# Kernel optimization log

Measured on AMD Instinct MI355X. Metric: run time of the kernel, lower is better.

Reference implementation:

```python
import jax, jax.numpy as jnp
import numpy as np

HIDDEN = 2048
HEADS = 16
HEAD_DIM = HIDDEN // HEADS          # 128
KV_RANK = HIDDEN // 8               # 256 (kv_compression_ratio = 8)
ATTN_DIM = HEADS * HEAD_DIM         # 2048
EPS = 1e-6


def setup_inputs() -> dict:
    key = jax.random.key(0)
    ks = jax.random.split(key, 6)
    B, L = 2, 2048
    x = jax.random.normal(ks[0], (B, L, HIDDEN), dtype=jnp.float32)
    # weights stored [in, out] (torch Linear applies x @ W.T; same math)
    s = lambda fan_in: 1.0 / np.sqrt(fan_in)
    Wq = jax.random.normal(ks[1], (HIDDEN, ATTN_DIM), dtype=jnp.float32) * s(HIDDEN)
    Wkv_down = jax.random.normal(ks[2], (HIDDEN, KV_RANK), dtype=jnp.float32) * s(HIDDEN)
    kv_norm_w = jnp.ones((KV_RANK,), dtype=jnp.float32)
    Wkv_up = jax.random.normal(ks[3], (KV_RANK, 2 * ATTN_DIM), dtype=jnp.float32) * s(KV_RANK)
    Wo = jax.random.normal(ks[4], (ATTN_DIM, HIDDEN), dtype=jnp.float32) * s(ATTN_DIM)
    return {"x": x, "Wq": Wq, "Wkv_down": Wkv_down, "kv_norm_w": kv_norm_w,
            "Wkv_up": Wkv_up, "Wo": Wo}


def rms_norm(x, w):
    ms = jnp.mean(x * x, axis=-1, keepdims=True)
    return w * (x * jax.lax.rsqrt(ms + EPS))


def reference(x, Wq, Wkv_down, kv_norm_w, Wkv_up, Wo):
    B, L, D = x.shape
    q = (x @ Wq).reshape(B, L, HEADS, HEAD_DIM)
    latent = rms_norm(x @ Wkv_down, kv_norm_w)            # [B, L, KV_RANK]
    kv = latent @ Wkv_up                                   # [B, L, 2*ATTN_DIM]
    k, v = jnp.split(kv, 2, axis=-1)
    k = k.reshape(B, L, HEADS, HEAD_DIM)
    v = v.reshape(B, L, HEADS, HEAD_DIM)
    scores = jnp.einsum('bxhd,byhd->bhxy', q, k) / np.sqrt(HEAD_DIM)
    causal = jnp.tril(jnp.ones((L, L), dtype=bool))
    scores = jnp.where(causal, scores, -jnp.inf)
    attn = jax.nn.softmax(scores, axis=-1)
    out = jnp.einsum('bhxy,byhd->bxhd', attn, v).reshape(B, L, ATTN_DIM)
    return out @ Wo
```

## Files before the change

### kernel.cpp

```cpp
#include <hip/hip_runtime.h>
#include <cstdint>
#include <cstddef>

typedef unsigned short u16;
typedef __bf16 bf16x8 __attribute__((ext_vector_type(8)));
typedef __bf16 bf16x2 __attribute__((ext_vector_type(2)));
typedef float f32x4 __attribute__((ext_vector_type(4)));
typedef uint32_t u32x4 __attribute__((ext_vector_type(4)));

__device__ inline u16 f2bf(float f) {
  uint32_t u = __builtin_bit_cast(uint32_t, f);
  u += 0x7fffu + ((u >> 16) & 1u);
  return (u16)(u >> 16);
}

#if defined(__has_builtin)
#if __has_builtin(__builtin_amdgcn_cvt_pk_bf16_f32)
#define HAVE_PK_BF16 1
#endif
#if __has_builtin(__builtin_amdgcn_exp2f)
#define EXP2(x) __builtin_amdgcn_exp2f(x)
#endif
#endif
#ifndef EXP2
#define EXP2(x) exp2f(x)
#endif

__device__ inline uint32_t pk2bf(float a, float b) {
#ifdef HAVE_PK_BF16
  bf16x2 v = __builtin_amdgcn_cvt_pk_bf16_f32(a, b);
  return __builtin_bit_cast(uint32_t, v);
#else
  return (uint32_t)f2bf(a) | ((uint32_t)f2bf(b) << 16);
#endif
}

__device__ inline f32x4 mfma16(bf16x8 a, bf16x8 b, f32x4 c) {
  return __builtin_amdgcn_mfma_f32_16x16x32_bf16(a, b, c, 0, 0, 0);
}

__device__ inline void gl_lds16(const u16* g, u16* l) {
  __builtin_amdgcn_global_load_lds(
      (const __attribute__((address_space(1))) uint32_t*)g,
      (__attribute__((address_space(3))) uint32_t*)l, 16, 0, 0);
}

__device__ void tcvt_dev(const float* __restrict__ in, u16* __restrict__ out,
                         int R, int C, int bx, int by, float (*t)[33], int tid) {
  int cb = bx * 32, rb = by * 32;
  int x = tid & 31, y = tid >> 5;
#pragma unroll
  for (int k = 0; k < 4; ++k)
    t[y + k * 8][x] = in[(size_t)(rb + y + k * 8) * C + cb + x];
  __syncthreads();
#pragma unroll
  for (int k = 0; k < 4; ++k)
    out[(size_t)(cb + y + k * 8) * R + rb + x] = f2bf(t[x][y + k * 8]);
}

__global__ __launch_bounds__(256) void k_prep(
    const float* __restrict__ x, const float* __restrict__ Wq,
    const float* __restrict__ Wkvd, const float* __restrict__ Wkvu,
    const float* __restrict__ Wo, u16* __restrict__ xbf,
    u16* __restrict__ WqkdT, u16* __restrict__ WkvuT, u16* __restrict__ WoT) {
  __shared__ float t[32][33];
  int bid = blockIdx.x, tid = threadIdx.x;
  if (bid < 8192) {
    int i = bid * 256 + tid;
    const float4 v = ((const float4*)x)[i];
    ushort4 o;
    o.x = f2bf(v.x); o.y = f2bf(v.y); o.z = f2bf(v.z); o.w = f2bf(v.w);
    ((ushort4*)xbf)[i] = o;
  } else if (bid < 12288) {
    int q = bid - 8192;
    tcvt_dev(Wq, WqkdT, 2048, 2048, q & 63, q >> 6, t, tid);
  } else if (bid < 12800) {
    int q = bid - 12288;
    tcvt_dev(Wkvd, WqkdT + 2048 * 2048, 2048, 256, q & 7, q >> 3, t, tid);
  } else if (bid < 13824) {
    int q = bid - 12800;
    tcvt_dev(Wkvu, WkvuT, 256, 4096, q & 127, q >> 7, t, tid);
  } else {
    int q = bid - 13824;
    tcvt_dev(Wo, WoT, 2048, 2048, q & 63, q >> 6, t, tid);
  }
}

__global__ __launch_bounds__(256) void k_rmsn(const u16* __restrict__ qc,
                                              const float* __restrict__ w,
                                              u16* __restrict__ out) {
  int row = blockIdx.x * 4 + (threadIdx.x >> 6);
  int lane = threadIdx.x & 63;
  const ushort4 u = *(const ushort4*)(qc + (size_t)row * 2304 + 2048 + lane * 4);
  float4 v;
  v.x = __builtin_bit_cast(float, (uint32_t)u.x << 16);
  v.y = __builtin_bit_cast(float, (uint32_t)u.y << 16);
  v.z = __builtin_bit_cast(float, (uint32_t)u.z << 16);
  v.w = __builtin_bit_cast(float, (uint32_t)u.w << 16);
  float ss = v.x * v.x + v.y * v.y + v.z * v.z + v.w * v.w;
#pragma unroll
  for (int off = 1; off < 64; off <<= 1) ss += __shfl_xor(ss, off);
  float r = rsqrtf(ss * (1.f / 256.f) + 1e-6f);
  const float4 wv = ((const float4*)w)[lane];
  ushort4 o;
  o.x = f2bf(v.x * r * wv.x);
  o.y = f2bf(v.y * r * wv.y);
  o.z = f2bf(v.z * r * wv.z);
  o.w = f2bf(v.w * r * wv.w);
  *(ushort4*)(out + (size_t)row * 256 + lane * 4) = o;
}

template <int BK, int MODE>
__global__ __launch_bounds__(256) void k_gemm(const u16* __restrict__ A,
                                              const u16* __restrict__ BT,
                                              void* __restrict__ C,
                                              u16* __restrict__ C2, int K,
                                              int ldc, float scale) {
  __shared__ __align__(16) u16 As[128 * BK];
  __shared__ __align__(16) u16 Bs[128 * BK];
  const int tid = threadIdx.x, wave = tid >> 6, lane = tid & 63;
  const int lanem = lane & 15, quad = lane >> 4;
  const int m0 = blockIdx.x * 128, n0 = blockIdx.y * 128;
  const int wr = wave >> 1, wc = wave & 1;
  f32x4 acc[4][4] = {};
  for (int k0 = 0; k0 < K; k0 += BK) {
    __syncthreads();
    if constexpr (BK == 32) {
      const int srow = lane >> 2, scol = (lane & 3) * 8;
#pragma unroll
      for (int c = 0; c < 2; ++c) {
        int p = wave * 2 + c;
        gl_lds16(A + (size_t)(m0 + p * 16 + srow) * K + k0 + scol, &As[p * 512]);
        gl_lds16(BT + (size_t)(n0 + p * 16 + srow) * K + k0 + scol, &Bs[p * 512]);
      }
    } else {
      const int srow = lane >> 3;
      const int scol = ((lane & 7) ^ srow) * 8;
#pragma unroll
      for (int c = 0; c < 4; ++c) {
        int p = wave * 4 + c;
        gl_lds16(A + (size_t)(m0 + p * 8 + srow) * K + k0 + scol, &As[p * 512]);
        gl_lds16(BT + (size_t)(n0 + p * 8 + srow) * K + k0 + scol, &Bs[p * 512]);
      }
    }
    __syncthreads();
#pragma unroll
    for (int kk = 0; kk < BK / 32; ++kk) {
      bf16x8 af[4], bff[4];
      if constexpr (BK == 32) {
#pragma unroll
        for (int i = 0; i < 4; ++i)
          af[i] = *(const bf16x8*)&As[(wr * 64 + i * 16 + lanem) * 32 + quad * 8];
#pragma unroll
        for (int j = 0; j < 4; ++j)
          bff[j] = *(const bf16x8*)&Bs[(wc * 64 + j * 16 + lanem) * 32 + quad * 8];
      } else {
        const int kp = ((kk * 4 + quad) ^ (lanem & 7)) << 3;
#pragma unroll
        for (int i = 0; i < 4; ++i)
          af[i] = *(const bf16x8*)&As[(wr * 64 + i * 16 + lanem) * 64 + kp];
#pragma unroll
        for (int j = 0; j < 4; ++j)
          bff[j] = *(const bf16x8*)&Bs[(wc * 64 + j * 16 + lanem) * 64 + kp];
      }
#pragma unroll
      for (int i = 0; i < 4; ++i)
#pragma unroll
        for (int j = 0; j < 4; ++j)
          acc[i][j] = mfma16(af[i], bff[j], acc[i][j]);
    }
  }
#pragma unroll
  for (int i = 0; i < 4; ++i)
#pragma unroll
    for (int j = 0; j < 4; ++j) {
      const int row0 = m0 + wr * 64 + i * 16 + quad * 4;
      const int col = n0 + wc * 64 + j * 16 + lanem;
      if constexpr (MODE == 2) {
        if (col >= 2048) {
          int cc = col - 2048, hh = cc >> 7, dd = cc & 127;
          int bb = row0 >> 11, ll = row0 & 2047;
          ushort4 pk;
          pk.x = f2bf(acc[i][j][0]);
          pk.y = f2bf(acc[i][j][1]);
          pk.z = f2bf(acc[i][j][2]);
          pk.w = f2bf(acc[i][j][3]);
          *(ushort4*)&C2[((size_t)(bb * 16 + hh) * 128 + dd) * 2048 + ll] = pk;
          continue;
        }
      }
#pragma unroll
      for (int r = 0; r < 4; ++r) {
        float v = acc[i][j][r] * scale;
        if constexpr (MODE == 0)
          ((float*)C)[(size_t)(row0 + r) * ldc + col] = v;
        else if constexpr (MODE == 1)
          ((u16*)C)[(size_t)(row0 + r) * ldc + col] = f2bf(v);
        else
          ((u16*)C)[(size_t)(row0 + r) * 2048 + col] = f2bf(v);
      }
    }
}

__global__ __launch_bounds__(256) void k_attn(const u16* __restrict__ qg,
                                              const u16* __restrict__ kg,
                                              const u16* __restrict__ vtg,
                                              u16* __restrict__ ao) {
  __shared__ __align__(16) u16 Ks[2][64 * 128];
  __shared__ __align__(16) u16 VTs[2][144 * 64];
  const int bid = blockIdx.x;
  const int p = bid >> 5, u = bid & 31;
  const int qt = (bid < 256) ? (15 - p) : (p - 8);
  const int bh = (u & 7) * 4 + (u >> 3);
  const int b = bh >> 4, h = bh & 15;
  const int tid = threadIdx.x, w = tid >> 6, lane = tid & 63;
  const int lanem = lane & 15, quad = lane >> 4;
  const int qb = qt * 128, nt = 2 * qt + 2;

  const int kr = lane >> 4, kc = lane & 15;
  const u16* kbp[4];
#pragma unroll
  for (int j = 0; j < 4; ++j) {
    int key = ((w >> 1) << 5) + (j << 3) + ((w & 1) << 2) + kr;
    kbp[j] = kg + (size_t)(b * 2048 + key) * 2048 + h * 128 +
             ((kc ^ (j * 4 + kr)) << 3);
  }
  const int vr = lane >> 3, vc = lane & 7;
  const u16* vbp[4];
#pragma unroll
  for (int j = 0; j < 4; ++j) {
    int row = w * 32 + j * 8 + vr;
    vbp[j] = vtg + (size_t)(bh * 128 + row) * 2048 + ((vc ^ vr) << 3);
  }

  bf16x8 qf[2][4];
#pragma unroll
  for (int g = 0; g < 2; ++g) {
    const u16* qp = qg +
                    (size_t)(b * 2048 + qb + w * 32 + g * 16 + lanem) * 2304 +
                    h * 128 + quad * 8;
#pragma unroll
    for (int c = 0; c < 4; ++c) qf[g][c] = *(const bf16x8*)(qp + c * 32);
  }
  f32x4 o[2][9] = {};

  int kpc[4], vposc[2];
#pragma unroll
  for (int c = 0; c < 4; ++c) kpc[c] = ((c * 4 + quad) ^ lanem) << 3;
#pragma unroll
  for (int kk = 0; kk < 2; ++kk)
    vposc[kk] = ((kk * 4 + quad) ^ (lanem & 7)) << 3;

#pragma unroll
  for (int j = 0; j < 4; ++j) gl_lds16(kbp[j], &Ks[0][(w * 16 + j * 4) * 128]);
#pragma unroll
  for (int j = 0; j < 4; ++j) gl_lds16(vbp[j], &VTs[0][(w * 32 + j * 8) * 64]);
#pragma unroll
  for (int j = 0; j < 4; ++j) { kbp[j] += 64 * 2048; vbp[j] += 64; }
  {
    const ushort4 ones4{0x3f80u, 0x3f80u, 0x3f80u, 0x3f80u};
    for (int i = tid; i < 512; i += 256) {
      int bufi = i >> 8, off = (i & 255) * 4;
      *(ushort4*)&VTs[bufi][128 * 64 + off] = ones4;
    }
  }

  for (int t = 0; t < nt; ++t) {
    __syncthreads();
    if (t + 1 < nt) {
      int nb = (t + 1) & 1;
#pragma unroll
      for (int j = 0; j < 4; ++j)
        gl_lds16(kbp[j], &Ks[nb][(w * 16 + j * 4) * 128]);
#pragma unroll
      for (int j = 0; j < 4; ++j)
        gl_lds16(vbp[j], &VTs[nb][(w * 32 + j * 8) * 64]);
#pragma unroll
      for (int j = 0; j < 4; ++j) { kbp[j] += 64 * 2048; vbp[j] += 64; }
    }
    const int buf = t & 1;
    const u16* ksb = &Ks[buf][lanem * 128];
    const u16* vsb = &VTs[buf][lanem * 64];
    f32x4 s[2][4] = {};
#pragma unroll
    for (int c = 0; c < 4; ++c) {
      const u16* ka = ksb + kpc[c];
#pragma unroll
      for (int ss = 0; ss < 4; ++ss) {
        bf16x8 kf = *(const bf16x8*)(ka + ss * 2048);
        s[0][ss] = mfma16(kf, qf[0][c], s[0][ss]);
        s[1][ss] = mfma16(kf, qf[1][c], s[1][ss]);
      }
    }
    if (t >= nt - 2) {
      const int krel = t * 64 - qb;
#pragma unroll
      for (int g = 0; g < 2; ++g) {
        const int qrow = w * 32 + g * 16 + lanem;
#pragma unroll
        for (int ss = 0; ss < 4; ++ss) {
          const int kb0 = krel + ((ss & 2) << 4) + ((ss & 1) << 2) + (quad << 3);
#pragma unroll
          for (int r = 0; r < 4; ++r)
            if (kb0 + r > qrow) s[g][ss][r] = -1e30f;
        }
      }
    }
    bf16x8 pf[2][2];
#pragma unroll
    for (int g = 0; g < 2; ++g)
#pragma unroll
      for (int f = 0; f < 2; ++f) {
        u32x4 pw;
        pw.x = pk2bf(EXP2(s[g][2 * f][0]), EXP2(s[g][2 * f][1]));
        pw.y = pk2bf(EXP2(s[g][2 * f][2]), EXP2(s[g][2 * f][3]));
        pw.z = pk2bf(EXP2(s[g][2 * f + 1][0]), EXP2(s[g][2 * f + 1][1]));
        pw.w = pk2bf(EXP2(s[g][2 * f + 1][2]), EXP2(s[g][2 * f + 1][3]));
        pf[g][f] = __builtin_bit_cast(bf16x8, pw);
      }
#pragma unroll
    for (int dc = 0; dc < 9; ++dc) {
      const u16* va = vsb + dc * 1024;
      bf16x8 vf0 = *(const bf16x8*)(va + vposc[0]);
      bf16x8 vf1 = *(const bf16x8*)(va + vposc[1]);
      o[0][dc] = mfma16(pf[0][0], vf0, o[0][dc]);
      o[0][dc] = mfma16(pf[0][1], vf1, o[0][dc]);
      o[1][dc] = mfma16(pf[1][0], vf0, o[1][dc]);
      o[1][dc] = mfma16(pf[1][1], vf1, o[1][dc]);
    }
  }
#pragma unroll
  for (int g = 0; g < 2; ++g)
#pragma unroll
    for (int r = 0; r < 4; ++r) {
      const float inv = 1.f / o[g][8][r];
      u16* op = ao +
                (size_t)(b * 2048 + qb + w * 32 + g * 16 + quad * 4 + r) * 2048 +
                h * 128;
#pragma unroll
      for (int dc = 0; dc < 8; ++dc)
        op[dc * 16 + lanem] = f2bf(o[g][dc][r] * inv);
    }
}

extern "C" void kernel_launch(void* const* d_in, const int* in_sizes, int n_in,
                              void* d_out, int out_size, void* d_ws, size_t ws_size,
                              hipStream_t stream) {
  const float* x    = (const float*)d_in[0];
  const float* Wq   = (const float*)d_in[1];
  const float* Wkvd = (const float*)d_in[2];
  const float* wn   = (const float*)d_in[3];
  const float* Wkvu = (const float*)d_in[4];
  const float* Wo   = (const float*)d_in[5];
  float* out = (float*)d_out;

  char* w0 = (char*)d_ws;
  u16* xbf   = (u16*)(w0);
  u16* qc    = (u16*)(w0 + 16777216);
  u16* WqkdT = (u16*)(w0 + 35651584);
  u16* WoT   = (u16*)(w0 + 45088768);
  u16* WkvuT = (u16*)(w0 + 53477376);
  u16* kbf   = (u16*)(w0 + 55574528);
  u16* vtbf  = (u16*)(w0 + 72351744);
  u16* latbf = WqkdT;
  u16* aobf  = xbf;

  const float sc2 = 0.08838834764831845f * 1.4426950408889634f;

  k_prep<<<17920, 256, 0, stream>>>(x, Wq, Wkvd, Wkvu, Wo, xbf, WqkdT, WkvuT, WoT);
  k_gemm<32, 1><<<dim3(32, 18), 256, 0, stream>>>(xbf, WqkdT, qc, nullptr, 2048,
                                                  2304, sc2);
  k_rmsn<<<1024, 256, 0, stream>>>(qc, wn, latbf);
  k_gemm<64, 2><<<dim3(32, 32), 256, 0, stream>>>(latbf, WkvuT, kbf, vtbf, 256,
                                                  0, 1.0f);
  k_attn<<<512, 256, 0, stream>>>(qc, kbf, vtbf, aobf);
  k_gemm<32, 0><<<dim3(32, 16), 256, 0, stream>>>(aobf, WoT, out, nullptr, 2048,
                                                  2048, 1.0f);
}
```

Before: 314.3 us.

## Split long causal attention query tiles across two key ranges with reduction kernel

The attention kernel now splits each of the 8 longest query tiles (qt 8..15) into two blocks that cover separate halves of the key range. Each half writes unnormalized fp32 partial outputs and row sums to a workspace, and a new reduction kernel adds them and normalizes into the bf16 attention output. This is meant to balance the load across CUs, since the longest causal tiles set the critical path of the 512-block grid. In exchange it adds a second launch and an fp32 partial write and read. The split path is used only if the workspace is large enough.

After: 326.5 us. 3.9% more time.

```diff
diff --git a/kernel.cpp b/kernel.cpp
--- a/kernel.cpp
+++ b/kernel.cpp
@@ -202,16 +202,43 @@
     }
 }
 
+template <bool SPLIT>
 __global__ __launch_bounds__(256) void k_attn(const u16* __restrict__ qg,
                                               const u16* __restrict__ kg,
                                               const u16* __restrict__ vtg,
-                                              u16* __restrict__ ao) {
+                                              u16* __restrict__ ao,
+                                              float* __restrict__ OP,
+                                              float* __restrict__ LP) {
   __shared__ __align__(16) u16 Ks[2][64 * 128];
   __shared__ __align__(16) u16 VTs[2][144 * 64];
   const int bid = blockIdx.x;
-  const int p = bid >> 5, u = bid & 31;
-  const int qt = (bid < 256) ? (15 - p) : (p - 8);
-  const int bh = (u & 7) * 4 + (u >> 3);
+  int qt, bh, ts, te, ck = 0;
+  bool part = false;
+  if constexpr (SPLIT) {
+    if (bid < 512) {
+      qt = 15 - (bid >> 6);
+      const int rem = bid & 63;
+      ck = rem & 1;
+      const int uu = rem >> 1;
+      bh = (uu & 7) * 4 + (uu >> 3);
+      ts = ck ? (qt + 1) : 0;
+      te = ck ? (2 * qt + 2) : (qt + 1);
+      part = true;
+    } else {
+      const int idx = bid - 512;
+      qt = 7 - (idx >> 5);
+      const int u = idx & 31;
+      bh = (u & 7) * 4 + (u >> 3);
+      ts = 0;
+      te = 2 * qt + 2;
+    }
+  } else {
+    const int p = bid >> 5, u = bid & 31;
+    qt = (bid < 256) ? (15 - p) : (p - 8);
+    bh = (u & 7) * 4 + (u >> 3);
+    ts = 0;
+    te = 2 * qt + 2;
+  }
   const int b = bh >> 4, h = bh & 15;
   const int tid = threadIdx.x, w = tid >> 6, lane = tid & 63;
   const int lanem = lane & 15, quad = lane >> 4;
@@ -223,14 +250,15 @@
   for (int j = 0; j < 4; ++j) {
     int key = ((w >> 1) << 5) + (j << 3) + ((w & 1) << 2) + kr;
     kbp[j] = kg + (size_t)(b * 2048 + key) * 2048 + h * 128 +
-             ((kc ^ (j * 4 + kr)) << 3);
+             ((kc ^ (j * 4 + kr)) << 3) + (size_t)ts * 64 * 2048;
   }
   const int vr = lane >> 3, vc = lane & 7;
   const u16* vbp[4];
 #pragma unroll
   for (int j = 0; j < 4; ++j) {
     int row = w * 32 + j * 8 + vr;
-    vbp[j] = vtg + (size_t)(bh * 128 + row) * 2048 + ((vc ^ vr) << 3);
+    vbp[j] = vtg + (size_t)(bh * 128 + row) * 2048 + ((vc ^ vr) << 3) +
+             (size_t)ts * 64;
   }
 
   bf16x8 qf[2][4];
@@ -265,10 +293,10 @@
     }
   }
 
-  for (int t = 0; t < nt; ++t) {
+  for (int t = ts; t < te; ++t) {
     __syncthreads();
-    if (t + 1 < nt) {
-      int nb = (t + 1) & 1;
+    if (t + 1 < te) {
+      int nb = (t + 1 - ts) & 1;
 #pragma unroll
       for (int j = 0; j < 4; ++j)
         gl_lds16(kbp[j], &Ks[nb][(w * 16 + j * 4) * 128]);
@@ -278,7 +306,7 @@
 #pragma unroll
       for (int j = 0; j < 4; ++j) { kbp[j] += 64 * 2048; vbp[j] += 64; }
     }
-    const int buf = t & 1;
+    const int buf = (t - ts) & 1;
     const u16* ksb = &Ks[buf][lanem * 128];
     const u16* vsb = &VTs[buf][lanem * 64];
     f32x4 s[2][4] = {};
@@ -329,18 +357,63 @@
       o[1][dc] = mfma16(pf[1][1], vf1, o[1][dc]);
     }
   }
-#pragma unroll
-  for (int g = 0; g < 2; ++g)
-#pragma unroll
-    for (int r = 0; r < 4; ++r) {
-      const float inv = 1.f / o[g][8][r];
-      u16* op = ao +
-                (size_t)(b * 2048 + qb + w * 32 + g * 16 + quad * 4 + r) * 2048 +
-                h * 128;
-#pragma unroll
-      for (int dc = 0; dc < 8; ++dc)
-        op[dc * 16 + lanem] = f2bf(o[g][dc][r] * inv);
-    }
+  if (SPLIT && part) {
+    const int slot = ((qt - 8) * 32 + bh) * 2 + ck;
+    float* op = OP + (size_t)slot * 16384;
+#pragma unroll
+    for (int g = 0; g < 2; ++g)
+#pragma unroll
+      for (int r = 0; r < 4; ++r) {
+        const int row = w * 32 + g * 16 + quad * 4 + r;
+#pragma unroll
+        for (int dc = 0; dc < 8; ++dc)
+          op[row * 128 + dc * 16 + lanem] = o[g][dc][r];
+        if (lanem == 0) LP[slot * 128 + row] = o[g][8][r];
+      }
+  } else {
+#pragma unroll
+    for (int g = 0; g < 2; ++g)
+#pragma unroll
+      for (int r = 0; r < 4; ++r) {
+        const float inv = 1.f / o[g][8][r];
+        u16* op = ao +
+                  (size_t)(b * 2048 + qb + w * 32 + g * 16 + quad * 4 + r) * 2048 +
+                  h * 128;
+#pragma unroll
+        for (int dc = 0; dc < 8; ++dc)
+          op[dc * 16 + lanem] = f2bf(o[g][dc][r] * inv);
+      }
+  }
+}
+
+__global__ __launch_bounds__(256) void k_ared(const float* __restrict__ OP,
+                                              const float* __restrict__ LP,
+                                              u16* __restrict__ ao) {
+  __shared__ float linv[128];
+  const int sp = blockIdx.x;
+  const int qt = 8 + (sp >> 5), bh = sp & 31;
+  const int b = bh >> 4, h = bh & 15;
+  const int tid = threadIdx.x;
+  if (tid < 128)
+    linv[tid] = 1.f / (LP[sp * 256 + tid] + LP[sp * 256 + 128 + tid]);
+  __syncthreads();
+  const float4* pa = (const float4*)(OP + (size_t)sp * 32768);
+  const float4* pb = pa + 4096;
+  u16* abase = ao + (size_t)(b * 2048 + qt * 128) * 2048 + h * 128;
+#pragma unroll
+  for (int k = 0; k < 16; ++k) {
+    const int fi = k * 256 + tid;
+    const int row = fi >> 5, dd = (fi & 31) * 4;
+    const float4 va = pa[fi];
+    const float4 vb = pb[fi];
+    const float inv = linv[row];
+    ushort4 o4;
+    o4.x = f2bf((va.x + vb.x) * inv);
+    o4.y = f2bf((va.y + vb.y) * inv);
+    o4.z = f2bf((va.z + vb.z) * inv);
+    o4.w = f2bf((va.w + vb.w) * inv);
+    *(ushort4*)(abase + (size_t)row * 2048 + dd) = o4;
+  }
 }
 
 extern "C" void kernel_launch(void* const* d_in, const int* in_sizes, int n_in,
@@ -365,6 +438,13 @@
   u16* latbf = WqkdT;
   u16* aobf  = xbf;
 
+  const size_t PBOFF = 89128960;
+  const size_t OPSZ  = 256ull * 2 * 128 * 128 * 4;
+  const size_t LPSZ  = 256ull * 2 * 128 * 4;
+  const bool do_split = ws_size >= PBOFF + OPSZ + LPSZ;
+  float* OP = (float*)(w0 + PBOFF);
+  float* LP = (float*)(w0 + PBOFF + OPSZ);
+
   const float sc2 = 0.08838834764831845f * 1.4426950408889634f;
 
   k_prep<<<17920, 256, 0, stream>>>(x, Wq, Wkvd, Wkvu, Wo, xbf, WqkdT, WkvuT, WoT);
@@ -373,7 +453,12 @@
   k_rmsn<<<1024, 256, 0, stream>>>(qc, wn, latbf);
   k_gemm<64, 2><<<dim3(32, 32), 256, 0, stream>>>(latbf, WkvuT, kbf, vtbf, 256,
                                                   0, 1.0f);
-  k_attn<<<512, 256, 0, stream>>>(qc, kbf, vtbf, aobf);
+  if (do_split) {
+    k_attn<true><<<768, 256, 0, stream>>>(qc, kbf, vtbf, aobf, OP, LP);
+    k_ared<<<256, 256, 0, stream>>>(OP, LP, aobf);
+  } else {
+    k_attn<false><<<512, 256, 0, stream>>>(qc, kbf, vtbf, aobf, nullptr, nullptr);
+  }
   k_gemm<32, 0><<<dim3(32, 16), 256, 0, stream>>>(aobf, WoT, out, nullptr, 2048,
                                                   2048, 1.0f);
 }
```

## Split causal attention along keys into two halves with a reduction kernel

Applied to the files above, without the earlier changes.

Adds a 512-thread attention kernel. Each block handles a 256-row query tile and half of the key range, and writes normalized partial outputs plus row sums to workspace. A second kernel combines the two halves weighted by their row sums. The aim is to balance the causal workload across blocks and raise occupancy, at the cost of an extra global round trip and launch. It also raises BK from 32 to 64 for the Q/latent and output GEMMs. The new path runs only when the workspace is large enough.

Result: slower. 395.2 us (+25.8%).

```diff
diff --git a/kernel.cpp b/kernel.cpp
--- a/kernel.cpp
+++ b/kernel.cpp
@@ -12,6 +12,9 @@
   uint32_t u = __builtin_bit_cast(uint32_t, f);
   u += 0x7fffu + ((u >> 16) & 1u);
   return (u16)(u >> 16);
+}
+__device__ inline float bf2f(u16 u) {
+  return __builtin_bit_cast(float, (uint32_t)u << 16);
 }
 
 #if defined(__has_builtin)
@@ -93,10 +96,7 @@
   int lane = threadIdx.x & 63;
   const ushort4 u = *(const ushort4*)(qc + (size_t)row * 2304 + 2048 + lane * 4);
   float4 v;
-  v.x = __builtin_bit_cast(float, (uint32_t)u.x << 16);
-  v.y = __builtin_bit_cast(float, (uint32_t)u.y << 16);
-  v.z = __builtin_bit_cast(float, (uint32_t)u.z << 16);
-  v.w = __builtin_bit_cast(float, (uint32_t)u.w << 16);
+  v.x = bf2f(u.x); v.y = bf2f(u.y); v.z = bf2f(u.z); v.w = bf2f(u.w);
   float ss = v.x * v.x + v.y * v.y + v.z * v.z + v.w * v.w;
 #pragma unroll
   for (int off = 1; off < 64; off <<= 1) ss += __shfl_xor(ss, off);
@@ -202,6 +202,194 @@
     }
 }
 
+__global__ __launch_bounds__(512, 4) void k_attn8(const u16* __restrict__ qg,
+                                                  const u16* __restrict__ kg,
+                                                  const u16* __restrict__ vtg,
+                                                  u16* __restrict__ OPb,
+                                                  float* __restrict__ LP) {
+  __shared__ __align__(16) u16 Ks[2][64 * 128];
+  __shared__ __align__(16) u16 VTs[2][144 * 64];
+  const int bid = blockIdx.x;
+  const int mq = (bid < 256) ? (7 - (bid >> 6)) : ((bid - 256) >> 6);
+  const int uu0 = bid & 63;
+  const int ck = uu0 & 1;
+  const int uu = uu0 >> 1;
+  const int bh = (uu & 7) * 4 + (uu >> 3);
+  const int b = bh >> 4, h = bh & 15;
+  const int ntile = 4 * mq + 4, half = 2 * mq + 2;
+  const int ts = ck ? half : 0;
+  const int te = ck ? ntile : half;
+  const int qb = mq * 256;
+
+  const int tid = threadIdx.x, w = tid >> 6, lane = tid & 63;
+  const int lanem = lane & 15, quad = lane >> 4;
+
+  const int kr = lane >> 4, kc = lane & 15;
+  const u16* kbp[2];
+  int kro[2];
+#pragma unroll
+  for (int j = 0; j < 2; ++j) {
+    const int rho = w * 8 + j * 4 + kr;
+    const int key = 32 * (rho >> 5) + 8 * ((rho >> 2) & 3) +
+                    4 * ((rho >> 4) & 1) + (rho & 3);
+    kbp[j] = kg + (size_t)(b * 2048 + key) * 2048 + h * 128 +
+             ((kc ^ (rho & 15)) << 3) + (size_t)ts * 64 * 2048;
+    kro[j] = rho * 128;
+  }
+  const int vr = lane >> 3, vc = lane & 7;
+  const u16* vbp[2];
+  int vro[2];
+#pragma unroll
+  for (int j = 0; j < 2; ++j) {
+    const int row = w * 16 + j * 8 + vr;
+    vbp[j] = vtg + (size_t)(bh * 128 + row) * 2048 + ((vc ^ vr) << 3) +
+             (size_t)ts * 64;
+    vro[j] = row * 64;
+  }
+
+  bf16x8 qf[2][4];
+#pragma unroll
+  for (int g = 0; g < 2; ++g) {
+    const u16* qp = qg +
+                    (size_t)(b * 2048 + qb + w * 32 + g * 16 + lanem) * 2304 +
+                    h * 128 + quad * 8;
+#pragma unroll
+    for (int c = 0; c < 4; ++c) qf[g][c] = *(const bf16x8*)(qp + c * 32);
+  }
+  f32x4 o[2][9] = {};
+
+  int kpc[4], vposc[2];
+#pragma unroll
+  for (int c = 0; c < 4; ++c) kpc[c] = ((c * 4 + quad) ^ lanem) << 3;
+#pragma unroll
+  for (int kk = 0; kk < 2; ++kk)
+    vposc[kk] = ((kk * 4 + quad) ^ (lanem & 7)) << 3;
+
+#pragma unroll
+  for (int j = 0; j < 2; ++j) gl_lds16(kbp[j], &Ks[0][kro[j]]);
+#pragma unroll
+  for (int j = 0; j < 2; ++j) gl_lds16(vbp[j], &VTs[0][vro[j]]);
+#pragma unroll
+  for (int j = 0; j < 2; ++j) { kbp[j] += 64 * 2048; vbp[j] += 64; }
+  {
+    const ushort4 ones4{0x3f80u, 0x3f80u, 0x3f80u, 0x3f80u};
+    const int bufi = tid >> 8, off = (tid & 255) * 4;
+    *(ushort4*)&VTs[bufi][128 * 64 + off] = ones4;
+  }
+
+  for (int t = ts; t < te; ++t) {
+    __syncthreads();
+    if (t + 1 < te) {
+      const int nb = (t + 1 - ts) & 1;
+#pragma unroll
+      for (int j = 0; j < 2; ++j) gl_lds16(kbp[j], &Ks[nb][kro[j]]);
+#pragma unroll
+      for (int j = 0; j < 2; ++j) gl_lds16(vbp[j], &VTs[nb][vro[j]]);
+#pragma unroll
+      for (int j = 0; j < 2; ++j) { kbp[j] += 64 * 2048; vbp[j] += 64; }
+    }
+    const int buf = (t - ts) & 1;
+    const u16* ksb = &Ks[buf][lanem * 128];
+    const u16* vsb = &VTs[buf][lanem * 64];
+    f32x4 s[2][4] = {};
+#pragma unroll
+    for (int c = 0; c < 4; ++c) {
+      const u16* ka = ksb + kpc[c];
+#pragma unroll
+      for (int ss = 0; ss < 4; ++ss) {
+        bf16x8 kf = *(const bf16x8*)(ka + ss * 2048);
+        s[0][ss] = mfma16(kf, qf[0][c], s[0][ss]);
+        s[1][ss] = mfma16(kf, qf[1][c], s[1][ss]);
+      }
+    }
+    if (t >= ntile - 4) {
+      const int krel = t * 64 - qb;
+#pragma unroll
+      for (int g = 0; g < 2; ++g) {
+        const int qrow = w * 32 + g * 16 + lanem;
+#pragma unroll
+        for (int ss = 0; ss < 4; ++ss) {
+          const int kb0 = krel + ((ss & 2) << 4) + ((ss & 1) << 2) + (quad << 3);
+#pragma unroll
+          for (int r = 0; r < 4; ++r)
+            if (kb0 + r > qrow) s[g][ss][r] = -1e30f;
+        }
+      }
+    }
+    bf16x8 pf[2][2];
+#pragma unroll
+    for (int g = 0; g < 2; ++g)
+#pragma unroll
+      for (int f = 0; f < 2; ++f) {
+        u32x4 pw;
+        pw.x = pk2bf(EXP2(s[g][2 * f][0]), EXP2(s[g][2 * f][1]));
+        pw.y = pk2bf(EXP2(s[g][2 * f][2]), EXP2(s[g][2 * f][3]));
+        pw.z = pk2bf(EXP2(s[g][2 * f + 1][0]), EXP2(s[g][2 * f + 1][1]));
+        pw.w = pk2bf(EXP2(s[g][2 * f + 1][2]), EXP2(s[g][2 * f + 1][3]));
+        pf[g][f] = __builtin_bit_cast(bf16x8, pw);
+      }
+#pragma unroll
+    for (int dc = 0; dc < 9; ++dc) {
+      const u16* va = vsb + dc * 1024;
+      bf16x8 vf0 = *(const bf16x8*)(va + vposc[0]);
+      bf16x8 vf1 = *(const bf16x8*)(va + vposc[1]);
+      o[0][dc] = mfma16(pf[0][0], vf0, o[0][dc]);
+      o[0][dc] = mfma16(pf[0][1], vf1, o[0][dc]);
+      o[1][dc] = mfma16(pf[1][0], vf0, o[1][dc]);
+      o[1][dc] = mfma16(pf[1][1], vf1, o[1][dc]);
+    }
+  }
+  const int slot = (mq * 32 + bh) * 2 + ck;
+  u16* opb = OPb + (size_t)slot * 32768;
+#pragma unroll
+  for (int g = 0; g < 2; ++g)
+#pragma unroll
+    for (int r = 0; r < 4; ++r) {
+      const int row = w * 32 + g * 16 + quad * 4 + r;
+      const float l = o[g][8][r];
+      const float inv = (l > 0.f) ? (1.f / l) : 0.f;
+#pragma unroll
+      for (int dc = 0; dc < 8; ++dc)
+        opb[row * 128 + dc * 16 + lanem] = f2bf(o[g][dc][r] * inv);
+      if (lanem == 0) LP[slot * 256 + row] = l;
+    }
+}
+
+__global__ __launch_bounds__(256) void k_ared2(const u16* __restrict__ OPb,
+                                               const float* __restrict__ LP,
+                                               u16* __restrict__ ao) {
+  __shared__ float2 wgt[256];
+  const int sp = blockIdx.x;
+  const int mq = sp >> 5, bh = sp & 31;
+  const int b = bh >> 4, h = bh & 15;
+  const int tid = threadIdx.x;
+  const int s0 = sp * 2, s1 = sp * 2 + 1;
+  {
+    const float l0 = LP[s0 * 256 + tid];
+    const float l1 = LP[s1 * 256 + tid];
+    const float inv = 1.f / (l0 + l1);
+    wgt[tid] = float2{l0 * inv, l1 * inv};
+  }
+  __syncthreads();
+  const ushort4* p0 = (const ushort4*)(OPb + (size_t)s0 * 32768);
+  const ushort4* p1 = (const ushort4*)(OPb + (size_t)s1 * 32768);
+  u16* abase = ao + (size_t)(b * 2048 + mq * 256) * 2048 + h * 128;
+#pragma unroll 4
+  for (int k = 0; k < 32; ++k) {
+    const int idx = k * 256 + tid;
+    const int row = idx >> 5, d4 = (idx & 31) * 4;
+    const ushort4 a4 = p0[idx];
+    const ushort4 b4 = p1[idx];
+    const float2 wv = wgt[row];
+    ushort4 o4;
+    o4.x = f2bf(bf2f(a4.x) * wv.x + bf2f(b4.x) * wv.y);
+    o4.y = f2bf(bf2f(a4.y) * wv.x + bf2f(b4.y) * wv.y);
+    o4.z = f2bf(bf2f(a4.z) * wv.x + bf2f(b4.z) * wv.y);
+    o4.w = f2bf(bf2f(a4.w) * wv.x + bf2f(b4.w) * wv.y);
+    *(ushort4*)(abase + (size_t)row * 2048 + d4) = o4;
+  }
+}
+
 __global__ __launch_bounds__(256) void k_attn(const u16* __restrict__ qg,
                                               const u16* __restrict__ kg,
                                               const u16* __restrict__ vtg,
@@ -216,7 +404,6 @@
   const int tid = threadIdx.x, w = tid >> 6, lane = tid & 63;
   const int lanem = lane & 15, quad = lane >> 4;
   const int qb = qt * 128, nt = 2 * qt + 2;
-
   const int kr = lane >> 4, kc = lane & 15;
   const u16* kbp[4];
 #pragma unroll
@@ -232,7 +419,6 @@
     int row = w * 32 + j * 8 + vr;
     vbp[j] = vtg + (size_t)(bh * 128 + row) * 2048 + ((vc ^ vr) << 3);
   }
-
   bf16x8 qf[2][4];
 #pragma unroll
   for (int g = 0; g < 2; ++g) {
@@ -243,14 +429,12 @@
     for (int c = 0; c < 4; ++c) qf[g][c] = *(const bf16x8*)(qp + c * 32);
   }
   f32x4 o[2][9] = {};
-
   int kpc[4], vposc[2];
 #pragma unroll
   for (int c = 0; c < 4; ++c) kpc[c] = ((c * 4 + quad) ^ lanem) << 3;
 #pragma unroll
   for (int kk = 0; kk < 2; ++kk)
     vposc[kk] = ((kk * 4 + quad) ^ (lanem & 7)) << 3;
-
 #pragma unroll
   for (int j = 0; j < 4; ++j) gl_lds16(kbp[j], &Ks[0][(w * 16 + j * 4) * 128]);
 #pragma unroll
@@ -264,7 +448,6 @@
       *(ushort4*)&VTs[bufi][128 * 64 + off] = ones4;
     }
   }
-
   for (int t = 0; t < nt; ++t) {
     __syncthreads();
     if (t + 1 < nt) {
@@ -365,15 +548,27 @@
   u16* latbf = WqkdT;
   u16* aobf  = xbf;
 
+  const size_t PBOFF = 89128960;
+  const size_t OPSZ  = 512ull * 256 * 128 * 2;
+  const size_t LPSZ  = 512ull * 256 * 4;
+  const bool do_split = ws_size >= PBOFF + OPSZ + LPSZ;
+  u16* OPb  = (u16*)(w0 + PBOFF);
+  float* LP = (float*)(w0 + PBOFF + OPSZ);
+
   const float sc2 = 0.08838834764831845f * 1.4426950408889634f;
 
   k_prep<<<17920, 256, 0, stream>>>(x, Wq, Wkvd, Wkvu, Wo, xbf, WqkdT, WkvuT, WoT);
-  k_gemm<32, 1><<<dim3(32, 18), 256, 0, stream>>>(xbf, WqkdT, qc, nullptr, 2048,
+  k_gemm<64, 1><<<dim3(32, 18), 256, 0, stream>>>(xbf, WqkdT, qc, nullptr, 2048,
                                                   2304, sc2);
   k_rmsn<<<1024, 256, 0, stream>>>(qc, wn, latbf);
   k_gemm<64, 2><<<dim3(32, 32), 256, 0, stream>>>(latbf, WkvuT, kbf, vtbf, 256,
                                                   0, 1.0f);
-  k_attn<<<512, 256, 0, stream>>>(qc, kbf, vtbf, aobf);
-  k_gemm<32, 0><<<dim3(32, 16), 256, 0, stream>>>(aobf, WoT, out, nullptr, 2048,
+  if (do_split) {
+    k_attn8<<<512, 512, 0, stream>>>(qc, kbf, vtbf, OPb, LP);
+    k_ared2<<<256, 256, 0, stream>>>(OPb, LP, aobf);
+  } else {
+    k_attn<<<512, 256, 0, stream>>>(qc, kbf, vtbf, aobf);
+  }
+  k_gemm<64, 0><<<dim3(32, 16), 256, 0, stream>>>(aobf, WoT, out, nullptr, 2048,
                                                   2048, 1.0f);
 }
```

## Split attention across 8 waves of 16 query rows and deepen GEMM K tiles

Applied to the files above, without the earlier changes.

The attention kernel now runs 512 threads (8 waves) per block, each wave owning 16 query rows instead of 32. Per-wave register state is halved and the K/V tile loads are spread over more threads. The aim is more waves in flight to hide LDS and exp latency, at the cost of each wave reusing every K/V fragment for fewer query rows. Separately, the Q/latent and output projection GEMMs switch from BK=32 to BK=64, cutting K-loop iterations and syncs but using more shared memory.

After: 286.0 us. 1.1x faster.

```diff
diff --git a/kernel.cpp b/kernel.cpp
--- a/kernel.cpp
+++ b/kernel.cpp
@@ -12,6 +12,9 @@
   uint32_t u = __builtin_bit_cast(uint32_t, f);
   u += 0x7fffu + ((u >> 16) & 1u);
   return (u16)(u >> 16);
+}
+__device__ inline float bf2f(u16 u) {
+  return __builtin_bit_cast(float, (uint32_t)u << 16);
 }
 
 #if defined(__has_builtin)
@@ -93,10 +96,7 @@
   int lane = threadIdx.x & 63;
   const ushort4 u = *(const ushort4*)(qc + (size_t)row * 2304 + 2048 + lane * 4);
   float4 v;
-  v.x = __builtin_bit_cast(float, (uint32_t)u.x << 16);
-  v.y = __builtin_bit_cast(float, (uint32_t)u.y << 16);
-  v.z = __builtin_bit_cast(float, (uint32_t)u.z << 16);
-  v.w = __builtin_bit_cast(float, (uint32_t)u.w << 16);
+  v.x = bf2f(u.x); v.y = bf2f(u.y); v.z = bf2f(u.z); v.w = bf2f(u.w);
   float ss = v.x * v.x + v.y * v.y + v.z * v.z + v.w * v.w;
 #pragma unroll
   for (int off = 1; off < 64; off <<= 1) ss += __shfl_xor(ss, off);
@@ -202,10 +202,10 @@
     }
 }
 
-__global__ __launch_bounds__(256) void k_attn(const u16* __restrict__ qg,
-                                              const u16* __restrict__ kg,
-                                              const u16* __restrict__ vtg,
-                                              u16* __restrict__ ao) {
+__global__ __launch_bounds__(512, 3) void k_attn16(const u16* __restrict__ qg,
+                                                   const u16* __restrict__ kg,
+                                                   const u16* __restrict__ vtg,
+                                                   u16* __restrict__ ao) {
   __shared__ __align__(16) u16 Ks[2][64 * 128];
   __shared__ __align__(16) u16 VTs[2][144 * 64];
   const int bid = blockIdx.x;
@@ -218,31 +218,31 @@
   const int qb = qt * 128, nt = 2 * qt + 2;
 
   const int kr = lane >> 4, kc = lane & 15;
-  const u16* kbp[4];
-#pragma unroll
-  for (int j = 0; j < 4; ++j) {
-    int key = ((w >> 1) << 5) + (j << 3) + ((w & 1) << 2) + kr;
+  const u16* kbp[2];
+#pragma unroll
+  for (int j = 0; j < 2; ++j) {
+    const int rho = w * 8 + j * 4 + kr;
+    const int key = 32 * (rho >> 5) + 8 * ((rho >> 2) & 3) +
+                    4 * ((rho >> 4) & 1) + (rho & 3);
     kbp[j] = kg + (size_t)(b * 2048 + key) * 2048 + h * 128 +
-             ((kc ^ (j * 4 + kr)) << 3);
+             ((kc ^ (rho & 15)) << 3);
   }
   const int vr = lane >> 3, vc = lane & 7;
-  const u16* vbp[4];
-#pragma unroll
-  for (int j = 0; j < 4; ++j) {
-    int row = w * 32 + j * 8 + vr;
+  const u16* vbp[2];
+#pragma unroll
+  for (int j = 0; j < 2; ++j) {
+    const int row = w * 16 + j * 8 + vr;
     vbp[j] = vtg + (size_t)(bh * 128 + row) * 2048 + ((vc ^ vr) << 3);
   }
 
-  bf16x8 qf[2][4];
-#pragma unroll
-  for (int g = 0; g < 2; ++g) {
-    const u16* qp = qg +
-                    (size_t)(b * 2048 + qb + w * 32 + g * 16 + lanem) * 2304 +
+  bf16x8 qf[4];
+  {
+    const u16* qp = qg + (size_t)(b * 2048 + qb + w * 16 + lanem) * 2304 +
                     h * 128 + quad * 8;
 #pragma unroll
-    for (int c = 0; c < 4; ++c) qf[g][c] = *(const bf16x8*)(qp + c * 32);
-  }
-  f32x4 o[2][9] = {};
+    for (int c = 0; c < 4; ++c) qf[c] = *(const bf16x8*)(qp + c * 32);
+  }
+  f32x4 o[9] = {};
 
   int kpc[4], vposc[2];
 #pragma unroll
@@ -252,95 +252,84 @@
     vposc[kk] = ((kk * 4 + quad) ^ (lanem & 7)) << 3;
 
 #pragma unroll
-  for (int j = 0; j < 4; ++j) gl_lds16(kbp[j], &Ks[0][(w * 16 + j * 4) * 128]);
-#pragma unroll
-  for (int j = 0; j < 4; ++j) gl_lds16(vbp[j], &VTs[0][(w * 32 + j * 8) * 64]);
-#pragma unroll
-  for (int j = 0; j < 4; ++j) { kbp[j] += 64 * 2048; vbp[j] += 64; }
+  for (int j = 0; j < 2; ++j)
+    gl_lds16(kbp[j], &Ks[0][(w * 8 + j * 4) * 128]);
+#pragma unroll
+  for (int j = 0; j < 2; ++j)
+    gl_lds16(vbp[j], &VTs[0][(w * 16 + j * 8) * 64]);
+#pragma unroll
+  for (int j = 0; j < 2; ++j) { kbp[j] += 64 * 2048; vbp[j] += 64; }
   {
     const ushort4 ones4{0x3f80u, 0x3f80u, 0x3f80u, 0x3f80u};
-    for (int i = tid; i < 512; i += 256) {
-      int bufi = i >> 8, off = (i & 255) * 4;
-      *(ushort4*)&VTs[bufi][128 * 64 + off] = ones4;
-    }
+    const int bufi = tid >> 8, off = (tid & 255) * 4;
+    *(ushort4*)&VTs[bufi][128 * 64 + off] = ones4;
   }
 
   for (int t = 0; t < nt; ++t) {
     __syncthreads();
     if (t + 1 < nt) {
-      int nb = (t + 1) & 1;
-#pragma unroll
-      for (int j = 0; j < 4; ++j)
-        gl_lds16(kbp[j], &Ks[nb][(w * 16 + j * 4) * 128]);
-#pragma unroll
-      for (int j = 0; j < 4; ++j)
-        gl_lds16(vbp[j], &VTs[nb][(w * 32 + j * 8) * 64]);
-#pragma unroll
-      for (int j = 0; j < 4; ++j) { kbp[j] += 64 * 2048; vbp[j] += 64; }
+      const int nb = (t + 1) & 1;
+#pragma unroll
+      for (int j = 0; j < 2; ++j)
+        gl_lds16(kbp[j], &Ks[nb][(w * 8 + j * 4) * 128]);
+#pragma unroll
+      for (int j = 0; j < 2; ++j)
+        gl_lds16(vbp[j], &VTs[nb][(w * 16 + j * 8) * 64]);
+#pragma unroll
+      for (int j = 0; j < 2; ++j) { kbp[j] += 64 * 2048; vbp[j] += 64; }
     }
     const int buf = t & 1;
     const u16* ksb = &Ks[buf][lanem * 128];
     const u16* vsb = &VTs[buf][lanem * 64];
-    f32x4 s[2][4] = {};
+    f32x4 s[4] = {};
 #pragma unroll
     for (int c = 0; c < 4; ++c) {
       const u16* ka = ksb + kpc[c];
 #pragma unroll
       for (int ss = 0; ss < 4; ++ss) {
         bf16x8 kf = *(const bf16x8*)(ka + ss * 2048);
-        s[0][ss] = mfma16(kf, qf[0][c], s[0][ss]);
-        s[1][ss] = mfma16(kf, qf[1][c], s[1][ss]);
+        s[ss] = mfma16(kf, qf[c], s[ss]);
       }
     }
     if (t >= nt - 2) {
       const int krel = t * 64 - qb;
-#pragma unroll
-      for (int g = 0; g < 2; ++g) {
-        const int qrow = w * 32 + g * 16 + lanem;
-#pragma unroll
-        for (int ss = 0; ss < 4; ++ss) {
-          const int kb0 = krel + ((ss & 2) << 4) + ((ss & 1) << 2) + (quad << 3);
-#pragma unroll
-          for (int r = 0; r < 4; ++r)
-            if (kb0 + r > qrow) s[g][ss][r] = -1e30f;
-        }
-      }
-    }
-    bf16x8 pf[2][2];
-#pragma unroll
-    for (int g = 0; g < 2; ++g)
-#pragma unroll
-      for (int f = 0; f < 2; ++f) {
-        u32x4 pw;
-        pw.x = pk2bf(EXP2(s[g][2 * f][0]), EXP2(s[g][2 * f][1]));
-        pw.y = pk2bf(EXP2(s[g][2 * f][2]), EXP2(s[g][2 * f][3]));
-        pw.z = pk2bf(EXP2(s[g][2 * f + 1][0]), EXP2(s[g][2 * f + 1][1]));
-        pw.w = pk2bf(EXP2(s[g][2 * f + 1][2]), EXP2(s[g][2 * f + 1][3]));
-        pf[g][f] = __builtin_bit_cast(bf16x8, pw);
-      }
+      const int qrow = w * 16 + lanem;
+#pragma unroll
+      for (int ss = 0; ss < 4; ++ss) {
+        const int kb0 = krel + ((ss & 2) << 4) + ((ss & 1) << 2) + (quad << 3);
+#pragma unroll
+        for (int r = 0; r < 4; ++r)
+          if (kb0 + r > qrow) s[ss][r] = -1e30f;
+      }
+    }
+    bf16x8 pf[2];
+#pragma unroll
+    for (int f = 0; f < 2; ++f) {
+      u32x4 pw;
+      pw.x = pk2bf(EXP2(s[2 * f][0]), EXP2(s[2 * f][1]));
+      pw.y = pk2bf(EXP2(s[2 * f][2]), EXP2(s[2 * f][3]));
+      pw.z = pk2bf(EXP2(s[2 * f + 1][0]), EXP2(s[2 * f + 1][1]));
+      pw.w = pk2bf(EXP2(s[2 * f + 1][2]), EXP2(s[2 * f + 1][3]));
+      pf[f] = __builtin_bit_cast(bf16x8, pw);
+    }
 #pragma unroll
     for (int dc = 0; dc < 9; ++dc) {
       const u16* va = vsb + dc * 1024;
       bf16x8 vf0 = *(const bf16x8*)(va + vposc[0]);
       bf16x8 vf1 = *(const bf16x8*)(va + vposc[1]);
-      o[0][dc] = mfma16(pf[0][0], vf0, o[0][dc]);
-      o[0][dc] = mfma16(pf[0][1], vf1, o[0][dc]);
-      o[1][dc] = mfma16(pf[1][0], vf0, o[1][dc]);
-      o[1][dc] = mfma16(pf[1][1], vf1, o[1][dc]);
-    }
-  }
-#pragma unroll
-  for (int g = 0; g < 2; ++g)
-#pragma unroll
-    for (int r = 0; r < 4; ++r) {
-      const float inv = 1.f / o[g][8][r];
-      u16* op = ao +
-                (size_t)(b * 2048 + qb + w * 32 + g * 16 + quad * 4 + r) * 2048 +
-                h * 128;
-#pragma unroll
-      for (int dc = 0; dc < 8; ++dc)
-        op[dc * 16 + lanem] = f2bf(o[g][dc][r] * inv);
-    }
+      o[dc] = mfma16(pf[0], vf0, o[dc]);
+      o[dc] = mfma16(pf[1], vf1, o[dc]);
+    }
+  }
+#pragma unroll
+  for (int r = 0; r < 4; ++r) {
+    const float inv = 1.f / o[8][r];
+    u16* op = ao +
+              (size_t)(b * 2048 + qb + w * 16 + quad * 4 + r) * 2048 + h * 128;
+#pragma unroll
+    for (int dc = 0; dc < 8; ++dc)
+      op[dc * 16 + lanem] = f2bf(o[dc][r] * inv);
+  }
 }
 
 extern "C" void kernel_launch(void* const* d_in, const int* in_sizes, int n_in,
@@ -368,12 +357,12 @@
   const float sc2 = 0.08838834764831845f * 1.4426950408889634f;
 
   k_prep<<<17920, 256, 0, stream>>>(x, Wq, Wkvd, Wkvu, Wo, xbf, WqkdT, WkvuT, WoT);
-  k_gemm<32, 1><<<dim3(32, 18), 256, 0, stream>>>(xbf, WqkdT, qc, nullptr, 2048,
+  k_gemm<64, 1><<<dim3(32, 18), 256, 0, stream>>>(xbf, WqkdT, qc, nullptr, 2048,
                                                   2304, sc2);
   k_rmsn<<<1024, 256, 0, stream>>>(qc, wn, latbf);
   k_gemm<64, 2><<<dim3(32, 32), 256, 0, stream>>>(latbf, WkvuT, kbf, vtbf, 256,
                                                   0, 1.0f);
-  k_attn<<<512, 256, 0, stream>>>(qc, kbf, vtbf, aobf);
-  k_gemm<32, 0><<<dim3(32, 16), 256, 0, stream>>>(aobf, WoT, out, nullptr, 2048,
+  k_attn16<<<512, 512, 0, stream>>>(qc, kbf, vtbf, aobf);
+  k_gemm<64, 0><<<dim3(32, 16), 256, 0, stream>>>(aobf, WoT, out, nullptr, 2048,
                                                   2048, 1.0f);
 }
```
